# Kernel optimization log

Hardware: AMD Instinct MI355X
Metric: run time of the kernel (lower is better)

The kernel has to match this reference:

```python
import jax, jax.numpy as jnp
import numpy as np

DIM = 768
HEADS = 16
HEAD_DIM = DIM // HEADS  # 48


def setup_inputs() -> dict:
    key = jax.random.key(0)
    ks = jax.random.split(key, 9)
    s = 1.0 / np.sqrt(DIM)
    inp = {
        "x": jax.random.normal(ks[0], (4, 2048, DIM), dtype=jnp.float32),
        "Wq": jax.random.uniform(ks[1], (DIM, DIM), jnp.float32, -s, s),
        "bq": jax.random.uniform(ks[2], (DIM,), jnp.float32, -s, s),
        "Wk": jax.random.uniform(ks[3], (DIM, DIM), jnp.float32, -s, s),
        "bk": jax.random.uniform(ks[4], (DIM,), jnp.float32, -s, s),
        "Wv": jax.random.uniform(ks[5], (DIM, DIM), jnp.float32, -s, s),
        "bv": jax.random.uniform(ks[6], (DIM,), jnp.float32, -s, s),
        "Wo": jax.random.uniform(ks[7], (DIM, DIM), jnp.float32, -s, s),
        "bo": jax.random.uniform(ks[8], (DIM,), jnp.float32, -s, s),
    }
    return inp


def reference(x, Wq, bq, Wk, bk, Wv, bv, Wo, bo):
    B, S, _ = x.shape
    # torch nn.Linear: y = x @ W.T + b
    q = x @ Wq.T + bq
    k = x @ Wk.T + bk
    v = x @ Wv.T + bv
    # split heads: (B, H, S, Dh)
    q = q.reshape(B, S, HEADS, HEAD_DIM).transpose(0, 2, 1, 3)
    k = k.reshape(B, S, HEADS, HEAD_DIM).transpose(0, 2, 1, 3)
    v = v.reshape(B, S, HEADS, HEAD_DIM).transpose(0, 2, 1, 3)
    score = jnp.einsum("bhqd,bhkd->bhqk", q, k) / jnp.sqrt(jnp.float32(HEAD_DIM))
    attn = jax.nn.softmax(score, axis=-1)
    out = jnp.einsum("bhqk,bhkd->bhqd", attn, v)
    out = out.transpose(0, 2, 1, 3).reshape(B, S, DIM)
    return out @ Wo.T + bo
```

## Files before the change

### kernel.cpp

```cpp
#include <hip/hip_runtime.h>

#define DIM 768
#define SEQ 2048
#define NB 4
#define NH 16
#define DH 48
#define DP 64
#define BHN (NB*NH)
#define MTOK (NB*SEQ)

typedef __attribute__((ext_vector_type(8))) short bf16x8;
typedef __attribute__((ext_vector_type(4))) float f32x4;
typedef __attribute__((ext_vector_type(4))) unsigned int u32x4;

__device__ __forceinline__ unsigned short f32_to_bf16(float f) {
    union { float f; unsigned int u; } v; v.f = f;
    unsigned int r = v.u + 0x7fff + ((v.u >> 16) & 1);
    return (unsigned short)(r >> 16);
}

#if __has_builtin(__builtin_amdgcn_exp2f)
#define EXP2F(x) __builtin_amdgcn_exp2f(x)
#else
#define EXP2F(x) exp2f(x)
#endif

#define GL_LDS16(g, l) __builtin_amdgcn_global_load_lds( \
    (const __attribute__((address_space(1))) void*)(g),  \
    (__attribute__((address_space(3))) void*)(l), 16, 0, 0)

__global__ void cvt_f32_bf16(const float* __restrict__ src, unsigned short* __restrict__ dst, int n) {
    int i = (blockIdx.x * blockDim.x + threadIdx.x) * 4;
    if (i + 3 < n) {
        const float4 v = *(const float4*)(src + i);
        ushort4 o;
        o.x = f32_to_bf16(v.x); o.y = f32_to_bf16(v.y);
        o.z = f32_to_bf16(v.z); o.w = f32_to_bf16(v.w);
        *(ushort4*)(dst + i) = o;
    }
}

__global__ void cvt4_f32_bf16(const float* __restrict__ a, const float* __restrict__ b,
                              const float* __restrict__ c, const float* __restrict__ d,
                              unsigned short* __restrict__ dst, int n_each) {
    const float* srcs[4] = {a, b, c, d};
    const float* src = srcs[blockIdx.y];
    unsigned short* out = dst + blockIdx.y * n_each;
    int i = (blockIdx.x * blockDim.x + threadIdx.x) * 4;
    if (i + 3 < n_each) {
        const float4 v = *(const float4*)(src + i);
        ushort4 o;
        o.x = f32_to_bf16(v.x); o.y = f32_to_bf16(v.y);
        o.z = f32_to_bf16(v.z); o.w = f32_to_bf16(v.w);
        *(ushort4*)(out + i) = o;
    }
}

#define BK 32

__global__ __launch_bounds__(256) void qkv_gemm(
    const unsigned short* __restrict__ xb,
    const unsigned short* __restrict__ wb,
    const float* __restrict__ bq, const float* __restrict__ bk, const float* __restrict__ bv,
    unsigned short* __restrict__ Qb, unsigned short* __restrict__ Kb, unsigned short* __restrict__ Vt)
{
    const int z = blockIdx.z;
    const unsigned short* W = wb + z * (DIM * DIM);
    const float* bias = (z == 0) ? bq : (z == 1) ? bk : bv;
    const int row0 = blockIdx.x * 128;
    const int col0 = blockIdx.y * 128;

    __shared__ __align__(16) short As[128 * BK];
    __shared__ __align__(16) short Bs[128 * BK];

    const int tid = threadIdx.x;
    const int lane = tid & 63;
    const int w = tid >> 6;
    const int wy = w >> 1, wx = w & 1;
    const int l15 = lane & 15, quad = lane >> 4;
    const int lr = lane >> 2;
    const int lco = (lane & 3) * 8;

    f32x4 acc[4][4];
    for (int mi = 0; mi < 4; ++mi) for (int ni = 0; ni < 4; ++ni)
        for (int r = 0; r < 4; ++r) acc[mi][ni][r] = 0.f;

    for (int kt = 0; kt < DIM / BK; ++kt) {
        #pragma unroll
        for (int j = 0; j < 2; ++j) {
            const int c = w * 2 + j;
            GL_LDS16(&xb[(row0 + c * 16 + lr) * DIM + kt * BK + lco], &As[c * 512]);
            GL_LDS16(&W [(col0 + c * 16 + lr) * DIM + kt * BK + lco], &Bs[c * 512]);
        }
        __syncthreads();
        bf16x8 af[4], bfr[4];
        #pragma unroll
        for (int mi = 0; mi < 4; ++mi)
            af[mi] = *(const bf16x8*)&As[(wy * 64 + mi * 16 + l15) * BK + quad * 8];
        #pragma unroll
        for (int ni = 0; ni < 4; ++ni)
            bfr[ni] = *(const bf16x8*)&Bs[(wx * 64 + ni * 16 + l15) * BK + quad * 8];
        #pragma unroll
        for (int mi = 0; mi < 4; ++mi)
            #pragma unroll
            for (int ni = 0; ni < 4; ++ni)
                acc[mi][ni] = __builtin_amdgcn_mfma_f32_16x16x32_bf16(af[mi], bfr[ni], acc[mi][ni], 0, 0, 0);
        __syncthreads();
    }

    const float qscale = 0.14433756729740643f * 1.4426950408889634f;
    #pragma unroll
    for (int mi = 0; mi < 4; ++mi) {
        #pragma unroll
        for (int ni = 0; ni < 4; ++ni) {
            #pragma unroll
            for (int r = 0; r < 4; ++r) {
                int row = row0 + wy * 64 + mi * 16 + quad * 4 + r;
                int col = col0 + wx * 64 + ni * 16 + l15;
                float v = acc[mi][ni][r] + bias[col];
                int b = row >> 11, s = row & 2047;
                int h = col / DH, d = col - h * DH;
                int bh = b * NH + h;
                if (z == 0)      Qb[(bh * SEQ + s) * DP + d] = f32_to_bf16(v * qscale);
                else if (z == 1) Kb[(bh * SEQ + s) * DP + d] = f32_to_bf16(v);
                else             Vt[(bh * DP + d) * SEQ + s] = f32_to_bf16(v);
            }
        }
    }
}

__global__ __launch_bounds__(256) void out_gemm(
    const unsigned short* __restrict__ ab,
    const unsigned short* __restrict__ Wo,
    const float* __restrict__ bo,
    float* __restrict__ out)
{
    const int row0 = blockIdx.x * 128;
    const int col0 = blockIdx.y * 128;

    __shared__ __align__(16) short As[128 * BK];
    __shared__ __align__(16) short Bs[128 * BK];

    const int tid = threadIdx.x;
    const int lane = tid & 63;
    const int w = tid >> 6;
    const int wy = w >> 1, wx = w & 1;
    const int l15 = lane & 15, quad = lane >> 4;
    const int lr = lane >> 2;
    const int lco = (lane & 3) * 8;

    f32x4 acc[4][4];
    for (int mi = 0; mi < 4; ++mi) for (int ni = 0; ni < 4; ++ni)
        for (int r = 0; r < 4; ++r) acc[mi][ni][r] = 0.f;

    for (int kt = 0; kt < DIM / BK; ++kt) {
        #pragma unroll
        for (int j = 0; j < 2; ++j) {
            const int c = w * 2 + j;
            GL_LDS16(&ab[(row0 + c * 16 + lr) * DIM + kt * BK + lco], &As[c * 512]);
            GL_LDS16(&Wo[(col0 + c * 16 + lr) * DIM + kt * BK + lco], &Bs[c * 512]);
        }
        __syncthreads();
        bf16x8 af[4], bfr[4];
        #pragma unroll
        for (int mi = 0; mi < 4; ++mi)
            af[mi] = *(const bf16x8*)&As[(wy * 64 + mi * 16 + l15) * BK + quad * 8];
        #pragma unroll
        for (int ni = 0; ni < 4; ++ni)
            bfr[ni] = *(const bf16x8*)&Bs[(wx * 64 + ni * 16 + l15) * BK + quad * 8];
        #pragma unroll
        for (int mi = 0; mi < 4; ++mi)
            #pragma unroll
            for (int ni = 0; ni < 4; ++ni)
                acc[mi][ni] = __builtin_amdgcn_mfma_f32_16x16x32_bf16(af[mi], bfr[ni], acc[mi][ni], 0, 0, 0);
        __syncthreads();
    }

    #pragma unroll
    for (int mi = 0; mi < 4; ++mi)
        #pragma unroll
        for (int ni = 0; ni < 4; ++ni)
            #pragma unroll
            for (int r = 0; r < 4; ++r) {
                int row = row0 + wy * 64 + mi * 16 + quad * 4 + r;
                int col = col0 + wx * 64 + ni * 16 + l15;
                out[row * DIM + col] = acc[mi][ni][r] + bo[col];
            }
}

__device__ __forceinline__ int keyperm(int a) {
    return (a & 32) + ((a & 12) << 1) + ((a & 16) >> 2) + (a & 3);
}

__global__ __launch_bounds__(256) void attn_kernel(
    const unsigned short* __restrict__ Qb,
    const unsigned short* __restrict__ Kb,
    const unsigned short* __restrict__ Vt,
    unsigned short* __restrict__ Ob)
{
    const int bh = blockIdx.y;
    const int tile = blockIdx.x;
    const int tid = threadIdx.x;
    const int w = tid >> 6;
    const int lane = tid & 63;
    const int l15 = lane & 15, quad = lane >> 4;

    const unsigned short* Qh = Qb + bh * SEQ * DP;
    const unsigned short* Kh = Kb + bh * SEQ * DP;
    const unsigned short* Vh = Vt + bh * DP * SEQ;
    const int q0 = tile * 128 + w * 32;

    __shared__ __align__(16) short Ks[64 * 64];
    __shared__ __align__(16) short Vs[48 * 64];

    bf16x8 aq[2][2];
    #pragma unroll
    for (int m = 0; m < 2; ++m)
        #pragma unroll
        for (int ks = 0; ks < 2; ++ks)
            aq[m][ks] = *(const bf16x8*)&Qh[(q0 + m * 16 + l15) * DP + ks * 32 + quad * 8];

    f32x4 o[2][3];
    #pragma unroll
    for (int m = 0; m < 2; ++m) for (int ni = 0; ni < 3; ++ni)
        for (int r = 0; r < 4; ++r) o[m][ni][r] = 0.f;
    float ls[2][4];
    #pragma unroll
    for (int m = 0; m < 2; ++m) for (int r = 0; r < 4; ++r) ls[m][r] = 0.f;

    const int sa = tid >> 3;
    const int sc_ = tid & 7;
    const int lc8 = (sc_ ^ (sa & 7)) * 8;
    const int ka0 = keyperm(sa), ka1 = keyperm(sa + 32);
    const int lds_w0 = sa * 64 + sc_ * 8;
    const int lds_w1 = (sa + 32) * 64 + sc_ * 8;
    const bool vsec = (tid < 128);

    bf16x8 kr0, kr1, vr0, vr1;
    kr0 = *(const bf16x8*)&Kh[ka0 * DP + lc8];
    kr1 = *(const bf16x8*)&Kh[ka1 * DP + lc8];
    vr0 = *(const bf16x8*)&Vh[sa * SEQ + lc8];
    if (vsec) vr1 = *(const bf16x8*)&Vh[(sa + 32) * SEQ + lc8];

    for (int kt = 0; kt < SEQ / 64; ++kt) {
        __syncthreads();
        *(bf16x8*)&Ks[lds_w0] = kr0;
        *(bf16x8*)&Ks[lds_w1] = kr1;
        *(bf16x8*)&Vs[lds_w0] = vr0;
        if (vsec) *(bf16x8*)&Vs[lds_w1] = vr1;
        if (kt + 1 < SEQ / 64) {
            const int k0n = (kt + 1) * 64;
            kr0 = *(const bf16x8*)&Kh[(k0n + ka0) * DP + lc8];
            kr1 = *(const bf16x8*)&Kh[(k0n + ka1) * DP + lc8];
            vr0 = *(const bf16x8*)&Vh[sa * SEQ + k0n + lc8];
            if (vsec) vr1 = *(const bf16x8*)&Vh[(sa + 32) * SEQ + k0n + lc8];
        }
        __syncthreads();

        f32x4 sc[2][4];
        #pragma unroll
        for (int m = 0; m < 2; ++m) for (int n = 0; n < 4; ++n)
            for (int r = 0; r < 4; ++r) sc[m][n][r] = 0.f;
        #pragma unroll
        for (int ks = 0; ks < 2; ++ks) {
            #pragma unroll
            for (int n = 0; n < 4; ++n) {
                bf16x8 ak = *(const bf16x8*)&Ks[(n * 16 + l15) * 64 + (((ks * 4 + quad) ^ (l15 & 7)) * 8)];
                sc[0][n] = __builtin_amdgcn_mfma_f32_16x16x32_bf16(ak, aq[0][ks], sc[0][n], 0, 0, 0);
                sc[1][n] = __builtin_amdgcn_mfma_f32_16x16x32_bf16(ak, aq[1][ks], sc[1][n], 0, 0, 0);
            }
        }

        bf16x8 av[2][3];
        #pragma unroll
        for (int ks = 0; ks < 2; ++ks)
            #pragma unroll
            for (int mt = 0; mt < 3; ++mt)
                av[ks][mt] = *(const bf16x8*)&Vs[(mt * 16 + l15) * 64 + (((ks * 4 + quad) ^ (l15 & 7)) * 8)];

        #pragma unroll
        for (int m = 0; m < 2; ++m) {
            union { u32x4 u; bf16x8 h; } bp[2];
            #pragma unroll
            for (int ks = 0; ks < 2; ++ks) {
                #pragma unroll
                for (int w2 = 0; w2 < 4; ++w2) {
                    const int j0 = 2 * w2, j1 = 2 * w2 + 1;
                    float p0 = EXP2F(sc[m][2 * ks + (j0 >> 2)][j0 & 3]);
                    float p1 = EXP2F(sc[m][2 * ks + (j1 >> 2)][j1 & 3]);
                    ls[m][w2] += (p0 + p1);
                    bp[ks].u[w2] = __builtin_amdgcn_perm(__float_as_uint(p1), __float_as_uint(p0), 0x07060302u);
                }
            }
            #pragma unroll
            for (int ks = 0; ks < 2; ++ks)
                #pragma unroll
                for (int mt = 0; mt < 3; ++mt)
                    o[m][mt] = __builtin_amdgcn_mfma_f32_16x16x32_bf16(av[ks][mt], bp[ks].h, o[m][mt], 0, 0, 0);
        }
    }

    const int b = bh >> 4, h = bh & 15;
    #pragma unroll
    for (int m = 0; m < 2; ++m) {
        float lsum = (ls[m][0] + ls[m][1]) + (ls[m][2] + ls[m][3]);
        lsum += __shfl_xor(lsum, 16);
        lsum += __shfl_xor(lsum, 32);
        float inv = 1.f / lsum;
        #pragma unroll
        for (int mt = 0; mt < 3; ++mt)
            #pragma unroll
            for (int r = 0; r < 4; ++r) {
                int token = b * SEQ + q0 + m * 16 + l15;
                int d = mt * 16 + quad * 4 + r;
                Ob[token * DIM + h * DH + d] = f32_to_bf16(o[m][mt][r] * inv);
            }
    }
}

extern "C" void kernel_launch(void* const* d_in, const int* in_sizes, int n_in,
                              void* d_out, int out_size, void* d_ws, size_t ws_size,
                              hipStream_t stream) {
    const float* x  = (const float*)d_in[0];
    const float* Wq = (const float*)d_in[1]; const float* bq = (const float*)d_in[2];
    const float* Wk = (const float*)d_in[3]; const float* bk = (const float*)d_in[4];
    const float* Wv = (const float*)d_in[5]; const float* bv = (const float*)d_in[6];
    const float* Wo = (const float*)d_in[7]; const float* bo = (const float*)d_in[8];

    unsigned char* ws = (unsigned char*)d_ws;
    unsigned short* xb = (unsigned short*)(ws);
    unsigned short* wb = (unsigned short*)(ws + 12582912);
    unsigned short* Qb = (unsigned short*)(ws + 17301504);
    unsigned short* Kb = (unsigned short*)(ws + 34078720);
    unsigned short* Vt = (unsigned short*)(ws + 50855936);
    unsigned short* Ob = (unsigned short*)(ws + 67633152);

    hipMemsetAsync(Qb, 0, 16777216u, stream);

    cvt_f32_bf16<<<6144, 256, 0, stream>>>(x, xb, MTOK * DIM);
    cvt4_f32_bf16<<<dim3(576, 4), 256, 0, stream>>>(Wq, Wk, Wv, Wo, wb, DIM * DIM);

    qkv_gemm<<<dim3(MTOK / 128, DIM / 128, 3), 256, 0, stream>>>(xb, wb, bq, bk, bv, Qb, Kb, Vt);
    attn_kernel<<<dim3(SEQ / 128, BHN), 256, 0, stream>>>(Qb, Kb, Vt, Ob);
    out_gemm<<<dim3(MTOK / 128, DIM / 128), 256, 0, stream>>>(Ob, wb + 3 * DIM * DIM, bo, (float*)d_out);
}
```

Before: 241.5 us.

## Use 512-thread attention blocks, vectorize V-transpose stores, drop padding memset

The attention kernel now runs 8 waves per block over 256 queries, so each K/V tile staged in LDS is shared by twice as many waves and each thread issues fewer staging loads. Because the padded Q/K columns are no longer zeroed by a memset, the upper half of the second Q k-slice is zeroed in registers instead. The score MFMAs are reordered so all K fragments are loaded first and the first MFMA starts from a zero constant. The V-transposed epilogue in the QKV GEMM now packs four consecutive sequence values into a single 8-byte store. The risk is that padding columns of K now hold whatever was left in the workspace, which is only safe if the zeroed Q lanes mask every garbage term, including NaN values.

```diff
diff --git a/kernel.cpp b/kernel.cpp
--- a/kernel.cpp
+++ b/kernel.cpp
@@ -109,21 +109,40 @@
     }
 
     const float qscale = 0.14433756729740643f * 1.4426950408889634f;
-    #pragma unroll
-    for (int mi = 0; mi < 4; ++mi) {
-        #pragma unroll
-        for (int ni = 0; ni < 4; ++ni) {
-            #pragma unroll
-            for (int r = 0; r < 4; ++r) {
-                int row = row0 + wy * 64 + mi * 16 + quad * 4 + r;
+
+    if (z == 2) {
+        #pragma unroll
+        for (int mi = 0; mi < 4; ++mi) {
+            #pragma unroll
+            for (int ni = 0; ni < 4; ++ni) {
                 int col = col0 + wx * 64 + ni * 16 + l15;
-                float v = acc[mi][ni][r] + bias[col];
+                int h = col / DH, d = col - h * DH;
+                int row = row0 + wy * 64 + mi * 16 + quad * 4;
                 int b = row >> 11, s = row & 2047;
-                int h = col / DH, d = col - h * DH;
-                int bh = b * NH + h;
-                if (z == 0)      Qb[(bh * SEQ + s) * DP + d] = f32_to_bf16(v * qscale);
-                else if (z == 1) Kb[(bh * SEQ + s) * DP + d] = f32_to_bf16(v);
-                else             Vt[(bh * DP + d) * SEQ + s] = f32_to_bf16(v);
+                float bi = bias[col];
+                union { ushort4 v; unsigned short e[4]; } pk;
+                #pragma unroll
+                for (int r = 0; r < 4; ++r)
+                    pk.e[r] = f32_to_bf16(acc[mi][ni][r] + bi);
+                *(ushort4*)&Vt[((b * NH + h) * DP + d) * SEQ + s] = pk.v;
+            }
+        }
+    } else {
+        #pragma unroll
+        for (int mi = 0; mi < 4; ++mi) {
+            #pragma unroll
+            for (int ni = 0; ni < 4; ++ni) {
+                #pragma unroll
+                for (int r = 0; r < 4; ++r) {
+                    int row = row0 + wy * 64 + mi * 16 + quad * 4 + r;
+                    int col = col0 + wx * 64 + ni * 16 + l15;
+                    float v = acc[mi][ni][r] + bias[col];
+                    int b = row >> 11, s = row & 2047;
+                    int h = col / DH, d = col - h * DH;
+                    int bh = b * NH + h;
+                    if (z == 0) Qb[(bh * SEQ + s) * DP + d] = f32_to_bf16(v * qscale);
+                    else        Kb[(bh * SEQ + s) * DP + d] = f32_to_bf16(v);
+                }
             }
         }
     }
@@ -192,7 +211,7 @@
     return (a & 32) + ((a & 12) << 1) + ((a & 16) >> 2) + (a & 3);
 }
 
-__global__ __launch_bounds__(256) void attn_kernel(
+__global__ __launch_bounds__(512, 4) void attn_kernel(
     const unsigned short* __restrict__ Qb,
     const unsigned short* __restrict__ Kb,
     const unsigned short* __restrict__ Vt,
@@ -208,7 +227,7 @@
     const unsigned short* Qh = Qb + bh * SEQ * DP;
     const unsigned short* Kh = Kb + bh * SEQ * DP;
     const unsigned short* Vh = Vt + bh * DP * SEQ;
-    const int q0 = tile * 128 + w * 32;
+    const int q0 = tile * 256 + w * 32;
 
     __shared__ __align__(16) short Ks[64 * 64];
     __shared__ __align__(16) short Vs[48 * 64];
@@ -219,6 +238,11 @@
         #pragma unroll
         for (int ks = 0; ks < 2; ++ks)
             aq[m][ks] = *(const bf16x8*)&Qh[(q0 + m * 16 + l15) * DP + ks * 32 + quad * 8];
+    if (quad >= 2) {
+        const bf16x8 z8 = {0, 0, 0, 0, 0, 0, 0, 0};
+        aq[0][1] = z8;
+        aq[1][1] = z8;
+    }
 
     f32x4 o[2][3];
     #pragma unroll
@@ -228,47 +252,46 @@
     #pragma unroll
     for (int m = 0; m < 2; ++m) for (int r = 0; r < 4; ++r) ls[m][r] = 0.f;
 
+    const f32x4 FZ = {0.f, 0.f, 0.f, 0.f};
+
     const int sa = tid >> 3;
     const int sc_ = tid & 7;
     const int lc8 = (sc_ ^ (sa & 7)) * 8;
-    const int ka0 = keyperm(sa), ka1 = keyperm(sa + 32);
-    const int lds_w0 = sa * 64 + sc_ * 8;
-    const int lds_w1 = (sa + 32) * 64 + sc_ * 8;
-    const bool vsec = (tid < 128);
-
-    bf16x8 kr0, kr1, vr0, vr1;
-    kr0 = *(const bf16x8*)&Kh[ka0 * DP + lc8];
-    kr1 = *(const bf16x8*)&Kh[ka1 * DP + lc8];
-    vr0 = *(const bf16x8*)&Vh[sa * SEQ + lc8];
-    if (vsec) vr1 = *(const bf16x8*)&Vh[(sa + 32) * SEQ + lc8];
+    const int ka = keyperm(sa);
+    const int lds_w = sa * 64 + sc_ * 8;
+    const bool vld = (sa < 48);
+
+    bf16x8 kr, vr;
+    kr = *(const bf16x8*)&Kh[ka * DP + lc8];
+    if (vld) vr = *(const bf16x8*)&Vh[sa * SEQ + lc8];
 
     for (int kt = 0; kt < SEQ / 64; ++kt) {
         __syncthreads();
-        *(bf16x8*)&Ks[lds_w0] = kr0;
-        *(bf16x8*)&Ks[lds_w1] = kr1;
-        *(bf16x8*)&Vs[lds_w0] = vr0;
-        if (vsec) *(bf16x8*)&Vs[lds_w1] = vr1;
+        *(bf16x8*)&Ks[lds_w] = kr;
+        if (vld) *(bf16x8*)&Vs[lds_w] = vr;
         if (kt + 1 < SEQ / 64) {
             const int k0n = (kt + 1) * 64;
-            kr0 = *(const bf16x8*)&Kh[(k0n + ka0) * DP + lc8];
-            kr1 = *(const bf16x8*)&Kh[(k0n + ka1) * DP + lc8];
-            vr0 = *(const bf16x8*)&Vh[sa * SEQ + k0n + lc8];
-            if (vsec) vr1 = *(const bf16x8*)&Vh[(sa + 32) * SEQ + k0n + lc8];
-        }
-        __syncthreads();
-
+            kr = *(const bf16x8*)&Kh[(k0n + ka) * DP + lc8];
+            if (vld) vr = *(const bf16x8*)&Vh[sa * SEQ + k0n + lc8];
+        }
+        __syncthreads();
+
+        bf16x8 ak0[4], ak1[4];
+        #pragma unroll
+        for (int n = 0; n < 4; ++n) {
+            ak0[n] = *(const bf16x8*)&Ks[(n * 16 + l15) * 64 + ((quad ^ (l15 & 7)) * 8)];
+            ak1[n] = *(const bf16x8*)&Ks[(n * 16 + l15) * 64 + (((4 + quad) ^ (l15 & 7)) * 8)];
+        }
         f32x4 sc[2][4];
         #pragma unroll
-        for (int m = 0; m < 2; ++m) for (int n = 0; n < 4; ++n)
-            for (int r = 0; r < 4; ++r) sc[m][n][r] = 0.f;
-        #pragma unroll
-        for (int ks = 0; ks < 2; ++ks) {
-            #pragma unroll
-            for (int n = 0; n < 4; ++n) {
-                bf16x8 ak = *(const bf16x8*)&Ks[(n * 16 + l15) * 64 + (((ks * 4 + quad) ^ (l15 & 7)) * 8)];
-                sc[0][n] = __builtin_amdgcn_mfma_f32_16x16x32_bf16(ak, aq[0][ks], sc[0][n], 0, 0, 0);
-                sc[1][n] = __builtin_amdgcn_mfma_f32_16x16x32_bf16(ak, aq[1][ks], sc[1][n], 0, 0, 0);
-            }
+        for (int n = 0; n < 4; ++n) {
+            sc[0][n] = __builtin_amdgcn_mfma_f32_16x16x32_bf16(ak0[n], aq[0][0], FZ, 0, 0, 0);
+            sc[1][n] = __builtin_amdgcn_mfma_f32_16x16x32_bf16(ak0[n], aq[1][0], FZ, 0, 0, 0);
+        }
+        #pragma unroll
+        for (int n = 0; n < 4; ++n) {
+            sc[0][n] = __builtin_amdgcn_mfma_f32_16x16x32_bf16(ak1[n], aq[0][1], sc[0][n], 0, 0, 0);
+            sc[1][n] = __builtin_amdgcn_mfma_f32_16x16x32_bf16(ak1[n], aq[1][1], sc[1][n], 0, 0, 0);
         }
 
         bf16x8 av[2][3];
@@ -335,12 +358,10 @@
     unsigned short* Vt = (unsigned short*)(ws + 50855936);
     unsigned short* Ob = (unsigned short*)(ws + 67633152);
 
-    hipMemsetAsync(Qb, 0, 16777216u, stream);
-
     cvt_f32_bf16<<<6144, 256, 0, stream>>>(x, xb, MTOK * DIM);
     cvt4_f32_bf16<<<dim3(576, 4), 256, 0, stream>>>(Wq, Wk, Wv, Wo, wb, DIM * DIM);
 
     qkv_gemm<<<dim3(MTOK / 128, DIM / 128, 3), 256, 0, stream>>>(xb, wb, bq, bk, bv, Qb, Kb, Vt);
-    attn_kernel<<<dim3(SEQ / 128, BHN), 256, 0, stream>>>(Qb, Kb, Vt, Ob);
+    attn_kernel<<<dim3(SEQ / 256, BHN), 512, 0, stream>>>(Qb, Kb, Vt, Ob);
     out_gemm<<<dim3(MTOK / 128, DIM / 128), 256, 0, stream>>>(Ob, wb + 3 * DIM * DIM, bo, (float*)d_out);
 }
```

After: 220.8 us. 8.6% less time.
